# Optimization experiments

Hardware: AMD Instinct MI355X
Metric: run time of the kernel (lower is better)

The kernel has to match this reference:

```python
import jax, jax.numpy as jnp
import numpy as np

N_HEAD = 16
NEG_INF = -1e9  # matches the original's -1000000000.0 mask fill


def setup_inputs() -> dict:
    key = jax.random.key(0)
    k1, k2, k3 = jax.random.split(key, 3)
    n_embd = 1024
    b, t = 2, 2048
    x = jax.random.normal(k1, (b, t, n_embd), dtype=jnp.float32)
    w_attn = jax.random.normal(k2, (n_embd, 3 * n_embd), dtype=jnp.float32) * 0.02
    b_attn = jnp.zeros((3 * n_embd,), dtype=jnp.float32)
    w_proj = jax.random.normal(k3, (n_embd, n_embd), dtype=jnp.float32) * 0.02
    b_proj = jnp.zeros((n_embd,), dtype=jnp.float32)
    return {"x": x, "w_attn": w_attn, "b_attn": b_attn, "w_proj": w_proj, "b_proj": b_proj}


def reference(x, w_attn, b_attn, w_proj, b_proj):
    b, t, c = x.shape
    hd = c // N_HEAD
    scale = 1.0 / np.sqrt(hd)
    qkv = x @ w_attn + b_attn                        # [b, t, 3c]
    q, k, v = jnp.split(qkv, 3, axis=-1)
    # split heads -> [b, nh, t, hd]
    def heads(z):
        return z.reshape(b, t, N_HEAD, hd).transpose(0, 2, 1, 3)
    q, k, v = heads(q), heads(k), heads(v)
    att = jnp.einsum('bhqd,bhkd->bhqk', q, k) * scale  # [b, nh, t, t]
    mask = jnp.tril(jnp.ones((t, t), dtype=bool))
    att = jnp.where(mask[None, None], att, jnp.float32(NEG_INF))
    att = jax.nn.softmax(att, axis=-1)
    y = jnp.einsum('bhqk,bhkd->bhqd', att, v)          # [b, nh, t, hd]
    y = y.transpose(0, 2, 1, 3).reshape(b, t, c)
    return y @ w_proj + b_proj
```

## Files before the change

### kernel.cpp

```cpp
#include <hip/hip_runtime.h>
#include <hip/hip_bf16.h>
#include <math.h>

typedef __attribute__((ext_vector_type(8))) short short8;
typedef __attribute__((ext_vector_type(4))) float f32x4;
typedef unsigned short u16;

static __device__ __forceinline__ u16 f2bf(float f) {
  union { float f; unsigned u; } v; v.f = f;
  unsigned r = v.u + 0x7fffu + ((v.u >> 16) & 1u);
  return (u16)(r >> 16);
}

static __device__ __forceinline__ float bf2f(u16 h) {
  union { unsigned u; float f; } v; v.u = ((unsigned)h) << 16;
  return v.f;
}

static __device__ __forceinline__ unsigned cvt_pk_bf16(float lo, float hi) {
  unsigned r;
  asm("v_cvt_pk_bf16_f32 %0, %1, %2" : "=v"(r) : "v"(lo), "v"(hi));
  return r;
}

static __device__ __forceinline__ void gload_lds16(const void* g, void* l) {
  __builtin_amdgcn_global_load_lds(
      (const __attribute__((address_space(1))) void*)g,
      (__attribute__((address_space(3))) void*)l, 16, 0, 0);
}

__device__ __forceinline__ void transpose_tile(const float* __restrict__ W,
                                               u16* __restrict__ WT,
                                               int ND, int KD, int c0, int k0,
                                               float (*tile)[65], int t) {
  const int lr = t >> 2;
  const int lc = (t & 3) * 16;
  const float* src = W + (size_t)(k0 + lr) * ND + c0 + lc;
#pragma unroll
  for (int i = 0; i < 16; i += 4) {
    float4 v = *(const float4*)(src + i);
    tile[lr][lc + i] = v.x; tile[lr][lc + i + 1] = v.y;
    tile[lr][lc + i + 2] = v.z; tile[lr][lc + i + 3] = v.w;
  }
  __syncthreads();
  unsigned pk[8];
#pragma unroll
  for (int j = 0; j < 8; ++j) {
    u16 lo = f2bf(tile[lc + 2 * j][lr]);
    u16 hi = f2bf(tile[lc + 2 * j + 1][lr]);
    pk[j] = lo | ((unsigned)hi << 16);
  }
  u16* dst = WT + (size_t)(c0 + lr) * KD + k0 + lc;
  *(uint4*)(dst) = make_uint4(pk[0], pk[1], pk[2], pk[3]);
  *(uint4*)(dst + 8) = make_uint4(pk[4], pk[5], pk[6], pk[7]);
}

__global__ __launch_bounds__(256) void fused_prologue(const float* __restrict__ x,
                                                      const float* __restrict__ w_attn,
                                                      const float* __restrict__ w_proj,
                                                      u16* __restrict__ xb,
                                                      u16* __restrict__ wTa,
                                                      u16* __restrict__ wTp) {
  __shared__ float tile[64][65];
  const int b = blockIdx.x;
  const int t = threadIdx.x;
  if (b < 2048) {
    const int i = (b * 256 + t) * 8;
    float4 a = *(const float4*)(x + i);
    float4 c = *(const float4*)(x + i + 4);
    uint4 pk;
    pk.x = f2bf(a.x) | ((unsigned)f2bf(a.y) << 16);
    pk.y = f2bf(a.z) | ((unsigned)f2bf(a.w) << 16);
    pk.z = f2bf(c.x) | ((unsigned)f2bf(c.y) << 16);
    pk.w = f2bf(c.z) | ((unsigned)f2bf(c.w) << 16);
    *(uint4*)(xb + i) = pk;
  } else if (b < 2816) {
    const int id = b - 2048;
    transpose_tile(w_attn, wTa, 3072, 1024, (id % 48) * 64, (id / 48) * 64, tile, t);
  } else {
    const int id = b - 2816;
    transpose_tile(w_proj, wTp, 1024, 1024, (id % 16) * 64, (id / 16) * 64, tile, t);
  }
}

template<int NSIZE, int MODE, int BN>
__global__ __launch_bounds__(256) void gemm_bt(const u16* __restrict__ A,
                                               const u16* __restrict__ Bt,
                                               const float* __restrict__ bias,
                                               u16* __restrict__ qb,
                                               u16* __restrict__ kb,
                                               u16* __restrict__ vb,
                                               float* __restrict__ outp) {
  constexpr int K = 1024;
  constexpr int NT = BN / 32;
  __shared__ u16 As[128 * 128];
  __shared__ u16 Bs[BN * 128];
  const int tid = threadIdx.x;
  const int lane = tid & 63;
  const int wid = tid >> 6;
  const int l15 = lane & 15;
  const int g4 = lane >> 4;
  const int wm = (wid >> 1) * 64;
  const int wn = (wid & 1) * (BN / 2);
  const int row0 = blockIdx.x * 128;
  const int col0 = blockIdx.y * BN;

  f32x4 acc[4][NT] = {};

  for (int kt = 0; kt < K / 128; ++kt) {
#pragma unroll
    for (int cc = 0; cc < 8; ++cc) {
      const int c = tid + cc * 256;
      const int row = c >> 4;
      const int ch = (c & 15) ^ (row & 15);
      gload_lds16(A + (size_t)(row0 + row) * K + kt * 128 + ch * 8, As + c * 8);
    }
#pragma unroll
    for (int cc = 0; cc < BN / 16; ++cc) {
      const int c = tid + cc * 256;
      const int row = c >> 4;
      const int ch = (c & 15) ^ (row & 15);
      gload_lds16(Bt + (size_t)(col0 + row) * K + kt * 128 + ch * 8, Bs + c * 8);
    }
    asm volatile("s_waitcnt vmcnt(0)" ::: "memory");
    __builtin_amdgcn_s_barrier();
    asm volatile("" ::: "memory");

#pragma unroll
    for (int ks = 0; ks < 4; ++ks) {
      short8 af[4], bf[NT];
      const int chB = (((ks * 4 + g4) ^ l15) & 15) << 4;
#pragma unroll
      for (int mt = 0; mt < 4; ++mt) {
        const int row = wm + mt * 16 + l15;
        af[mt] = *(const short8*)((const char*)As + row * 256 + chB);
      }
#pragma unroll
      for (int nt = 0; nt < NT; ++nt) {
        const int row = wn + nt * 16 + l15;
        bf[nt] = *(const short8*)((const char*)Bs + row * 256 + chB);
      }
#pragma unroll
      for (int mt = 0; mt < 4; ++mt)
#pragma unroll
        for (int nt = 0; nt < NT; ++nt)
          acc[mt][nt] = __builtin_amdgcn_mfma_f32_16x16x32_bf16(af[mt], bf[nt], acc[mt][nt], 0, 0, 0);
    }

    asm volatile("" ::: "memory");
    __builtin_amdgcn_s_barrier();
  }

#pragma unroll
  for (int nt = 0; nt < NT; ++nt) {
    const int col = col0 + wn + nt * 16 + l15;
    const float bv = bias[col];
    if (MODE == 0) {
      const int part = col >> 10;
      const int h = (col >> 6) & 15;
      const int d = col & 63;
      u16* dp = part == 0 ? qb : kb;
#pragma unroll
      for (int mt = 0; mt < 4; ++mt) {
        if (part == 2) {
          const int t0 = row0 + wm + mt * 16 + g4 * 4;
          const int bidx = t0 >> 11;
          const int tt = t0 & 2047;
          const unsigned lo = f2bf(acc[mt][nt][0] + bv) | ((unsigned)f2bf(acc[mt][nt][1] + bv) << 16);
          const unsigned hi = f2bf(acc[mt][nt][2] + bv) | ((unsigned)f2bf(acc[mt][nt][3] + bv) << 16);
          *(uint2*)&vb[((size_t)((bidx << 4) + h) * 64 + d) * 2048 + tt] = make_uint2(lo, hi);
        } else {
#pragma unroll
          for (int r = 0; r < 4; ++r) {
            const int row = row0 + wm + mt * 16 + g4 * 4 + r;
            const int bidx = row >> 11;
            const int tt = row & 2047;
            dp[((size_t)((bidx << 4) + h) * 2048 + tt) * 64 + d] = f2bf(acc[mt][nt][r] + bv);
          }
        }
      }
    } else {
#pragma unroll
      for (int mt = 0; mt < 4; ++mt) {
#pragma unroll
        for (int r = 0; r < 4; ++r) {
          const int row = row0 + wm + mt * 16 + g4 * 4 + r;
          outp[(size_t)row * NSIZE + col] = acc[mt][nt][r] + bv;
        }
      }
    }
  }
}

__global__ __launch_bounds__(256, 3) void attn_fwd(const u16* __restrict__ Qb,
                                                   const u16* __restrict__ Kb,
                                                   const u16* __restrict__ Vtb,
                                                   u16* __restrict__ Yb,
                                                   char* __restrict__ pb) {
  __shared__ u16 Ks[2][64 * 64];
  __shared__ u16 Vs[2][64 * 64];
  __shared__ u16 Ps[4][1024];
  const int bh = blockIdx.x;
  const int y = blockIdx.y;
  int j, c0t, c1t, chunk, split;
  if (y < 8)       { j = 8 + y;  c0t = 0;  c1t = 15;        chunk = 0; split = 1; }
  else if (y < 16) { j = 15 - y; c0t = 0;  c1t = 2 * j + 1; chunk = 0; split = 0; }
  else             { j = y - 8;  c0t = 16; c1t = 2 * j + 1; chunk = 1; split = 1; }
  const int q0 = j * 128;
  const int tid = threadIdx.x;
  const int lane = tid & 63;
  const int wid = tid >> 6;
  const int l15 = lane & 15;
  const int g4 = lane >> 4;
  const size_t bhq = (size_t)bh * 2048 * 64;
  const u16* Kbase = Kb + bhq;
  const u16* Vbase = Vtb + bhq;
  const float C2 = 0.18033688011112042f;
  u16* Pw = &Ps[wid][0];
  const int wrow0 = q0 + wid * 32;

  short8 ones;
#pragma unroll
  for (int i = 0; i < 8; ++i) ones[i] = (short)0x3F80;

  short8 qf[2][2];
#pragma unroll
  for (int g = 0; g < 2; ++g) {
    const u16* qp = Qb + bhq + (size_t)(wrow0 + g * 16 + l15) * 64 + g4 * 8;
    qf[g][0] = *(const short8*)(qp);
    qf[g][1] = *(const short8*)(qp + 32);
  }
  f32x4 accy[2][4] = {};
  float m_q[2] = {-1e30f, -1e30f};
  float m_r[2][4] = {{-1e30f, -1e30f, -1e30f, -1e30f}, {-1e30f, -1e30f, -1e30f, -1e30f}};
  float l_r[2][4] = {};

  int cur = 0;
#pragma unroll
  for (int cc = 0; cc < 2; ++cc) {
    const int c = tid + cc * 256;
    const int srow = c >> 3;
    const int sblk = (c & 7) ^ (srow & 7);
    gload_lds16(Kbase + (size_t)(c0t * 64 + srow) * 64 + sblk * 8, Ks[0] + c * 8);
    gload_lds16(Vbase + (size_t)srow * 2048 + c0t * 64 + sblk * 8, Vs[0] + c * 8);
  }

  for (int kv = c0t; kv <= c1t; ++kv) {
    const int kv0 = kv * 64;
    if (kv < c1t) {
      const int nx0 = kv0 + 64;
#pragma unroll
      for (int cc = 0; cc < 2; ++cc) {
        const int c = tid + cc * 256;
        const int srow = c >> 3;
        const int sblk = (c & 7) ^ (srow & 7);
        gload_lds16(Kbase + (size_t)(nx0 + srow) * 64 + sblk * 8, Ks[cur ^ 1] + c * 8);
        gload_lds16(Vbase + (size_t)srow * 2048 + nx0 + sblk * 8, Vs[cur ^ 1] + c * 8);
      }
      asm volatile("s_waitcnt vmcnt(4)" ::: "memory");
    } else {
      asm volatile("s_waitcnt vmcnt(0)" ::: "memory");
    }
    __builtin_amdgcn_s_barrier();
    asm volatile("" ::: "memory");

    if (kv0 <= wrow0 + 31) {
      const u16* Kt = Ks[cur];
      const u16* Vt = Vs[cur];

      f32x4 s[2][4];
#pragma unroll
      for (int nt = 0; nt < 4; ++nt) {
        const int R = nt * 16 + l15;
        const int sw = (R & 7) << 4;
        short8 kf0 = *(const short8*)((const char*)Kt + R * 128 + ((g4 * 16) ^ sw));
        short8 kf1 = *(const short8*)((const char*)Kt + R * 128 + ((64 + g4 * 16) ^ sw));
        f32x4 z0 = __builtin_amdgcn_mfma_f32_16x16x32_bf16(kf0, qf[0][0], f32x4{}, 0, 0, 0);
        s[0][nt] = __builtin_amdgcn_mfma_f32_16x16x32_bf16(kf1, qf[0][1], z0, 0, 0, 0);
        f32x4 z1 = __builtin_amdgcn_mfma_f32_16x16x32_bf16(kf0, qf[1][0], f32x4{}, 0, 0, 0);
        s[1][nt] = __builtin_amdgcn_mfma_f32_16x16x32_bf16(kf1, qf[1][1], z1, 0, 0, 0);
      }

      short8 pf[2][2];
#pragma unroll
      for (int g = 0; g < 2; ++g) {
        const int grow0 = wrow0 + g * 16;
        if (kv0 + 63 > grow0) {
          const int qg = grow0 + l15;
#pragma unroll
          for (int nt = 0; nt < 4; ++nt) {
            const int kbase = kv0 + nt * 16 + g4 * 4;
#pragma unroll
            for (int r = 0; r < 4; ++r)
              if (kbase + r > qg) s[g][nt][r] = -1e30f;
          }
        }
        float mx = fmaxf(s[g][0][0], s[g][0][1]);
        mx = fmaxf(fmaxf(mx, s[g][0][2]), s[g][0][3]);
        mx = fmaxf(fmaxf(mx, s[g][1][0]), s[g][1][1]);
        mx = fmaxf(fmaxf(mx, s[g][1][2]), s[g][1][3]);
        mx = fmaxf(fmaxf(mx, s[g][2][0]), s[g][2][1]);
        mx = fmaxf(fmaxf(mx, s[g][2][2]), s[g][2][3]);
        mx = fmaxf(fmaxf(mx, s[g][3][0]), s[g][3][1]);
        mx = fmaxf(fmaxf(mx, s[g][3][2]), s[g][3][3]);
        mx = fmaxf(mx, __shfl_xor(mx, 16));
        mx = fmaxf(mx, __shfl_xor(mx, 32));
        if (!__all(mx <= m_q[g] + 44.0f)) {
          m_q[g] = fmaxf(m_q[g], mx);
#pragma unroll
          for (int rr = 0; rr < 4; ++rr) {
            const float mn = __shfl(m_q[g], g4 * 4 + rr);
            const float al = __builtin_amdgcn_exp2f((m_r[g][rr] - mn) * C2);
            m_r[g][rr] = mn;
            l_r[g][rr] *= al;
#pragma unroll
            for (int nt = 0; nt < 4; ++nt) accy[g][nt][rr] *= al;
          }
        }
        const float m2 = m_q[g] * C2;
#pragma unroll
        for (int nt = 0; nt < 4; ++nt)
#pragma unroll
          for (int r = 0; r < 4; ++r)
            s[g][nt][r] = __builtin_amdgcn_exp2f(fmaf(s[g][nt][r], C2, -m2));

#pragma unroll
        for (int nt = 0; nt < 4; ++nt) {
          const unsigned lo = cvt_pk_bf16(s[g][nt][0], s[g][nt][1]);
          const unsigned hi = cvt_pk_bf16(s[g][nt][2], s[g][nt][3]);
          const int colB = nt * 32 + g4 * 8;
          *(uint2*)((char*)Pw + l15 * 128 + (colB ^ ((l15 & 7) << 4))) = make_uint2(lo, hi);
        }
        {
          const int sw = (l15 & 7) << 4;
          pf[g][0] = *(const short8*)((const char*)Pw + l15 * 128 + ((g4 * 16) ^ sw));
          pf[g][1] = *(const short8*)((const char*)Pw + l15 * 128 + ((64 + g4 * 16) ^ sw));
        }
      }

#pragma unroll
      for (int g = 0; g < 2; ++g) {
        f32x4 ps = __builtin_amdgcn_mfma_f32_16x16x32_bf16(pf[g][0], ones, f32x4{}, 0, 0, 0);
        ps = __builtin_amdgcn_mfma_f32_16x16x32_bf16(pf[g][1], ones, ps, 0, 0, 0);
#pragma unroll
        for (int rr = 0; rr < 4; ++rr) l_r[g][rr] += ps[rr];
      }
#pragma unroll
      for (int nt = 0; nt < 4; ++nt) {
        const int R = nt * 16 + l15;
        const int sw = (R & 7) << 4;
        short8 vf0 = *(const short8*)((const char*)Vt + R * 128 + ((g4 * 16) ^ sw));
        short8 vf1 = *(const short8*)((const char*)Vt + R * 128 + ((64 + g4 * 16) ^ sw));
#pragma unroll
        for (int g = 0; g < 2; ++g) {
          accy[g][nt] = __builtin_amdgcn_mfma_f32_16x16x32_bf16(pf[g][0], vf0, accy[g][nt], 0, 0, 0);
          accy[g][nt] = __builtin_amdgcn_mfma_f32_16x16x32_bf16(pf[g][1], vf1, accy[g][nt], 0, 0, 0);
        }
      }
    }

    asm volatile("" ::: "memory");
    __builtin_amdgcn_s_barrier();
    cur ^= 1;
  }

  if (!split) {
#pragma unroll
    for (int g = 0; g < 2; ++g)
#pragma unroll
      for (int r = 0; r < 4; ++r) {
        const int row = wrow0 + g * 16 + g4 * 4 + r;
        const float inv = 1.0f / l_r[g][r];
        const size_t base = ((size_t)(bh >> 4) * 2048 + row) * 1024 + (bh & 15) * 64;
#pragma unroll
        for (int nt = 0; nt < 4; ++nt)
          Yb[base + nt * 16 + l15] = f2bf(accy[g][nt][r] * inv);
      }
  } else {
    char* slot = pb + ((size_t)(bh * 8 + (j - 8)) * 2 + chunk) * 17408;
    u16* O = (u16*)slot;
    float* mf = (float*)(slot + 16384);
    float* lf = (float*)(slot + 16896);
#pragma unroll
    for (int g = 0; g < 2; ++g)
#pragma unroll
      for (int r = 0; r < 4; ++r) {
        const int row = wid * 32 + g * 16 + g4 * 4 + r;
        const float inv = 1.0f / l_r[g][r];
#pragma unroll
        for (int nt = 0; nt < 4; ++nt)
          O[row * 64 + nt * 16 + l15] = f2bf(accy[g][nt][r] * inv);
        if (l15 == 0) { mf[row] = m_r[g][r]; lf[row] = l_r[g][r]; }
      }
  }
}

__global__ __launch_bounds__(256) void attn_combine(const char* __restrict__ pb,
                                                    u16* __restrict__ Yb) {
  const int x = blockIdx.x;
  const int bh = blockIdx.y;
  const int j = 8 + (x >> 1);
  const int half = x & 1;
  const int T = 2 * j + half;
  const char* s0 = pb + ((size_t)(bh * 8 + (j - 8)) * 2) * 17408;
  const char* s1 = s0 + 17408;
  const int tid = threadIdx.x;
  const int r64 = tid >> 2;
  const int rowl = half * 64 + r64;
  const int dc = (tid & 3) * 16;
  const float C2 = 0.18033688011112042f;
  const float m0 = ((const float*)(s0 + 16384))[rowl];
  const float m1 = ((const float*)(s1 + 16384))[rowl];
  const float l0 = ((const float*)(s0 + 16896))[rowl];
  const float l1 = ((const float*)(s1 + 16896))[rowl];
  const float m = fmaxf(m0, m1);
  const float w0 = __builtin_amdgcn_exp2f((m0 - m) * C2) * l0;
  const float w1 = __builtin_amdgcn_exp2f((m1 - m) * C2) * l1;
  const float inv = 1.0f / (w0 + w1);
  const float a0 = w0 * inv, a1 = w1 * inv;
  const u16* O0 = (const u16*)s0 + rowl * 64 + dc;
  const u16* O1 = (const u16*)s1 + rowl * 64 + dc;
  const int qrow = T * 64 + r64;
  u16* yp = Yb + ((size_t)(bh >> 4) * 2048 + qrow) * 1024 + (bh & 15) * 64 + dc;
  union { uint4 v; u16 h[8]; } a[2], b[2], o[2];
  a[0].v = *(const uint4*)O0; a[1].v = *(const uint4*)(O0 + 8);
  b[0].v = *(const uint4*)O1; b[1].v = *(const uint4*)(O1 + 8);
#pragma unroll
  for (int jj = 0; jj < 2; ++jj)
#pragma unroll
    for (int i = 0; i < 8; ++i)
      o[jj].h[i] = f2bf(bf2f(a[jj].h[i]) * a0 + bf2f(b[jj].h[i]) * a1);
  *(uint4*)yp = o[0].v;
  *(uint4*)(yp + 8) = o[1].v;
}

extern "C" void kernel_launch(void* const* d_in, const int* in_sizes, int n_in,
                              void* d_out, int out_size, void* d_ws, size_t ws_size,
                              hipStream_t stream) {
  const float* x      = (const float*)d_in[0];
  const float* w_attn = (const float*)d_in[1];
  const float* b_attn = (const float*)d_in[2];
  const float* w_proj = (const float*)d_in[3];
  const float* b_proj = (const float*)d_in[4];
  float* out = (float*)d_out;
  char* ws = (char*)d_ws;

  u16* xb  = (u16*)(ws + (size_t)0);
  u16* wTa = (u16*)(ws + ((size_t)8  << 20));
  u16* wTp = (u16*)(ws + ((size_t)14 << 20));
  u16* qb  = (u16*)(ws + ((size_t)16 << 20));
  u16* kb  = (u16*)(ws + ((size_t)24 << 20));
  u16* vb  = (u16*)(ws + ((size_t)32 << 20));
  u16* yb  = (u16*)(ws + ((size_t)40 << 20));
  char* pb = ws;

  fused_prologue<<<3072, 256, 0, stream>>>(x, w_attn, w_proj, xb, wTa, wTp);
  gemm_bt<3072, 0, 64><<<dim3(32, 48), 256, 0, stream>>>(xb, wTa, b_attn, qb, kb, vb, nullptr);
  attn_fwd<<<dim3(32, 24), 256, 0, stream>>>(qb, kb, vb, yb, pb);
  attn_combine<<<dim3(16, 32), 256, 0, stream>>>(pb, yb);
  gemm_bt<1024, 1, 64><<<dim3(32, 16), 256, 0, stream>>>(yb, wTp, b_proj, nullptr, nullptr, nullptr, out);
}
```

Measured before the change: 106.3 us.

## Double-buffer GEMM LDS tiles with K=64 steps to overlap loads and MFMA

Splits the K loop of the bf16 GEMM into 64-wide steps with two LDS buffers, prefetching the next A/B tile with direct-to-LDS loads while MFMAs consume the current one, and waits with a partial vmcnt. The aim is to hide global memory latency, which was previously exposed because each iteration waited for all loads before computing. The cost is twice as many barriers per K and a hardcoded vmcnt literal that assumes BN=64. The XOR swizzle changes to 8 chunks per row.

```diff
diff --git a/kernel.cpp b/kernel.cpp
--- a/kernel.cpp
+++ b/kernel.cpp
@@ -93,53 +93,74 @@
                                                float* __restrict__ outp) {
   constexpr int K = 1024;
   constexpr int NT = BN / 32;
-  __shared__ u16 As[128 * 128];
-  __shared__ u16 Bs[BN * 128];
+  static_assert(BN == 64, "vmcnt literal assumes BN=64");
+  __shared__ u16 As[2][128 * 64];
+  __shared__ u16 Bs[2][64 * 64];
   const int tid = threadIdx.x;
   const int lane = tid & 63;
   const int wid = tid >> 6;
   const int l15 = lane & 15;
   const int g4 = lane >> 4;
   const int wm = (wid >> 1) * 64;
-  const int wn = (wid & 1) * (BN / 2);
+  const int wn = (wid & 1) * 32;
   const int row0 = blockIdx.x * 128;
   const int col0 = blockIdx.y * BN;
 
   f32x4 acc[4][NT] = {};
 
-  for (int kt = 0; kt < K / 128; ++kt) {
-#pragma unroll
-    for (int cc = 0; cc < 8; ++cc) {
-      const int c = tid + cc * 256;
-      const int row = c >> 4;
-      const int ch = (c & 15) ^ (row & 15);
-      gload_lds16(A + (size_t)(row0 + row) * K + kt * 128 + ch * 8, As + c * 8);
+#pragma unroll
+  for (int i = 0; i < 4; ++i) {
+    const int c = tid + i * 256;
+    const int row = c >> 3;
+    const int blk = (c & 7) ^ (row & 7);
+    gload_lds16(A + (size_t)(row0 + row) * K + blk * 8, As[0] + c * 8);
+  }
+#pragma unroll
+  for (int i = 0; i < 2; ++i) {
+    const int c = tid + i * 256;
+    const int row = c >> 3;
+    const int blk = (c & 7) ^ (row & 7);
+    gload_lds16(Bt + (size_t)(col0 + row) * K + blk * 8, Bs[0] + c * 8);
+  }
+
+  int cur = 0;
+  for (int kt = 0; kt < K / 64; ++kt) {
+    if (kt + 1 < K / 64) {
+      const int ko = (kt + 1) * 64;
+#pragma unroll
+      for (int i = 0; i < 4; ++i) {
+        const int c = tid + i * 256;
+        const int row = c >> 3;
+        const int blk = (c & 7) ^ (row & 7);
+        gload_lds16(A + (size_t)(row0 + row) * K + ko + blk * 8, As[cur ^ 1] + c * 8);
+      }
+#pragma unroll
+      for (int i = 0; i < 2; ++i) {
+        const int c = tid + i * 256;
+        const int row = c >> 3;
+        const int blk = (c & 7) ^ (row & 7);
+        gload_lds16(Bt + (size_t)(col0 + row) * K + ko + blk * 8, Bs[cur ^ 1] + c * 8);
+      }
+      asm volatile("s_waitcnt vmcnt(6)" ::: "memory");
+    } else {
+      asm volatile("s_waitcnt vmcnt(0)" ::: "memory");
     }
-#pragma unroll
-    for (int cc = 0; cc < BN / 16; ++cc) {
-      const int c = tid + cc * 256;
-      const int row = c >> 4;
-      const int ch = (c & 15) ^ (row & 15);
-      gload_lds16(Bt + (size_t)(col0 + row) * K + kt * 128 + ch * 8, Bs + c * 8);
-    }
-    asm volatile("s_waitcnt vmcnt(0)" ::: "memory");
     __builtin_amdgcn_s_barrier();
     asm volatile("" ::: "memory");
 
-#pragma unroll
-    for (int ks = 0; ks < 4; ++ks) {
+    const u16* Ac = As[cur];
+    const u16* Bc = Bs[cur];
+#pragma unroll
+    for (int ks = 0; ks < 2; ++ks) {
       short8 af[4], bf[NT];
-      const int chB = (((ks * 4 + g4) ^ l15) & 15) << 4;
-#pragma unroll
-      for (int mt = 0; mt < 4; ++mt) {
-        const int row = wm + mt * 16 + l15;
-        af[mt] = *(const short8*)((const char*)As + row * 256 + chB);
-      }
-#pragma unroll
-      for (int nt = 0; nt < NT; ++nt) {
-        const int row = wn + nt * 16 + l15;
-        bf[nt] = *(const short8*)((const char*)Bs + row * 256 + chB);
-      }
+      const int B = ks * 64 + g4 * 16;
+      const int sw = (l15 & 7) << 4;
+#pragma unroll
+      for (int mt = 0; mt < 4; ++mt)
+        af[mt] = *(const short8*)((const char*)Ac + (wm + mt * 16 + l15) * 128 + (B ^ sw));
+#pragma unroll
+      for (int nt = 0; nt < NT; ++nt)
+        bf[nt] = *(const short8*)((const char*)Bc + (wn + nt * 16 + l15) * 128 + (B ^ sw));
 #pragma unroll
       for (int mt = 0; mt < 4; ++mt)
 #pragma unroll
@@ -149,6 +170,7 @@
 
     asm volatile("" ::: "memory");
     __builtin_amdgcn_s_barrier();
+    cur ^= 1;
   }
 
 #pragma unroll
```

New measurement: 102.3 us, median of 2. 1.04x faster.
